# Kernel optimization log

Hardware: AMD Instinct MI355X
Metric: run time of the kernel (lower is better)

## Reference

```python
import jax, jax.numpy as jnp
import numpy as np

B, S, D_MODEL, NUM_HEADS, DFF = 4, 2048, 256, 8, 1024
DEPTH = D_MODEL // NUM_HEADS
EPS = 1e-6
LENGTH_SCALE = 1.0


def setup_inputs() -> dict:
    key = jax.random.key(0)
    ks = jax.random.split(key, 18)
    n = lambda k, shp, s=0.05: (jax.random.normal(k, shp, dtype=jnp.float32) * s)
    return {
        "x": jax.random.normal(ks[0], (B, S, D_MODEL), dtype=jnp.float32),
        "wq_w": n(ks[1], (D_MODEL, D_MODEL)), "wq_b": jnp.zeros((D_MODEL,), jnp.float32),
        "wk_w": n(ks[2], (D_MODEL, D_MODEL)), "wk_b": jnp.zeros((D_MODEL,), jnp.float32),
        "wv_w": n(ks[3], (D_MODEL, D_MODEL)), "wv_b": jnp.zeros((D_MODEL,), jnp.float32),
        "wo_w": n(ks[4], (D_MODEL, D_MODEL)), "wo_b": jnp.zeros((D_MODEL,), jnp.float32),
        "ffn1_w": n(ks[5], (D_MODEL, DFF)), "ffn1_b": jnp.zeros((DFF,), jnp.float32),
        "ffn2_w": n(ks[6], (DFF, D_MODEL)), "ffn2_b": jnp.zeros((D_MODEL,), jnp.float32),
        "ln1_g": jnp.ones((D_MODEL,), jnp.float32), "ln1_b": jnp.zeros((D_MODEL,), jnp.float32),
        "ln2_g": jnp.ones((D_MODEL,), jnp.float32), "ln2_b": jnp.zeros((D_MODEL,), jnp.float32),
    }


def _layernorm(x, g, b):
    mu = jnp.mean(x, axis=-1, keepdims=True)
    var = jnp.mean(jnp.square(x - mu), axis=-1, keepdims=True)
    return (x - mu) * jax.lax.rsqrt(var + EPS) * g + b


def _split_heads(t):
    # [B,S,D_MODEL] -> [B,H,S,depth]
    return t.reshape(B, S, NUM_HEADS, DEPTH).transpose(0, 2, 1, 3)


def _encoder_layer(x, wq_w, wq_b, wk_w, wk_b, wv_w, wv_b, wo_w, wo_b,
                   ffn1_w, ffn1_b, ffn2_w, ffn2_b, ln1_g, ln1_b, ln2_g, ln2_b):
    q = _split_heads(x @ wq_w + wq_b)
    k = _split_heads(x @ wk_w + wk_b)
    v = _split_heads(x @ wv_w + wv_b)
    # pairwise squared distances: ||q||^2 - 2 q.k + ||k||^2 -> [B,H,S,S]
    q2 = jnp.sum(q * q, axis=-1)  # [B,H,S]
    k2 = jnp.sum(k * k, axis=-1)  # [B,H,S]
    dists = q2[..., :, None] - 2.0 * jnp.einsum("bhqd,bhkd->bhqk", q, k) + k2[..., None, :]
    # exponentiated-quadratic kernel, then softmax over keys (mask=None)
    attn = jax.nn.softmax(jnp.exp(-0.5 * dists / (LENGTH_SCALE ** 2)), axis=-1)
    out = jnp.einsum("bhqk,bhkd->bhqd", attn, v)  # [B,H,S,depth]
    out = out.transpose(0, 2, 1, 3).reshape(B, S, D_MODEL)
    attn_out = out @ wo_w + wo_b
    # dropout is identity (training=False)
    out1 = _layernorm(x + attn_out, ln1_g, ln1_b)
    ffn = jax.nn.relu(out1 @ ffn1_w + ffn1_b) @ ffn2_w + ffn2_b
    return _layernorm(out1 + ffn, ln2_g, ln2_b)


def reference(x, wq_w, wq_b, wk_w, wk_b, wv_w, wv_b, wo_w, wo_b,
              ffn1_w, ffn1_b, ffn2_w, ffn2_b, ln1_g, ln1_b, ln2_g, ln2_b):
    return _encoder_layer(x, wq_w, wq_b, wk_w, wk_b, wv_w, wv_b, wo_w, wo_b,
                          ffn1_w, ffn1_b, ffn2_w, ffn2_b, ln1_g, ln1_b, ln2_g, ln2_b)
```

## Files before the change

### kernel.cpp

```cpp
#include <hip/hip_runtime.h>
#include <hip/hip_bf16.h>

#define SQL  2048
#define DM   256
#define LNEPS 1e-6f
#define NLOG2E_H (-0.72134752f)
#define LOG2E    (1.44269504f)

#define B_XB    (0ull)
#define B_QB    (4ull<<20)
#define B_KB    (8ull<<20)
#define B_VT    (12ull<<20)
#define B_CTX   (16ull<<20)
#define B_O1B   (20ull<<20)
#define B_O1F   (24ull<<20)
#define B_MID   (32ull<<20)
#define B_WQKVT (48ull<<20)
#define B_WOT   ((48ull<<20)+(512ull<<10))
#define B_W1T   (49ull<<20)
#define B_W2T   ((49ull<<20)+(512ull<<10))
#define B_BQKV  (50ull<<20)
#define B_HQ    ((50ull<<20)+(64ull<<10))
#define B_HK    ((50ull<<20)+(320ull<<10))
#define B_C2    (0ull)

typedef float  f32x16 __attribute__((ext_vector_type(16)));
typedef short  bf16x8 __attribute__((ext_vector_type(8)));
typedef int    i32x4  __attribute__((ext_vector_type(4)));
typedef int    i32x2  __attribute__((ext_vector_type(2)));

static __device__ __forceinline__ unsigned short bfu(float f){
    __hip_bfloat16 h = __float2bfloat16(f);
    return *reinterpret_cast<unsigned short*>(&h);
}
static __device__ __forceinline__ unsigned pk2(float a, float b){
    return (unsigned)bfu(a) | ((unsigned)bfu(b) << 16);
}
static __device__ __forceinline__ void glds16(const void* g, void* l){
    __builtin_amdgcn_global_load_lds((const __attribute__((address_space(1))) unsigned int*)g,
                                     (__attribute__((address_space(3))) unsigned int*)l, 16, 0, 0);
}

__global__ __launch_bounds__(256) void k_packall(
    const float* __restrict__ wq, const float* __restrict__ wk, const float* __restrict__ wv,
    const float* __restrict__ wo, const float* __restrict__ w1, const float* __restrict__ w2,
    const float* __restrict__ bq, const float* __restrict__ bk, const float* __restrict__ bv,
    const float* __restrict__ x,
    unsigned short* __restrict__ wqkvT, unsigned short* __restrict__ woT,
    unsigned short* __restrict__ w1T, unsigned short* __restrict__ w2T,
    float* __restrict__ bqkv, unsigned short* __restrict__ xb)
{
    __shared__ float tile[32][33];
    const int bid = blockIdx.x;
    const int t = threadIdx.x;
    if (bid < 768) {
        const float* W; unsigned short* Wt; int K, N, xk, yn;
        if (bid < 192) {
            int which = bid >> 6, local = bid & 63;
            W = (which == 0) ? wq : (which == 1 ? wk : wv);
            Wt = wqkvT + which * 65536; K = 256; N = 256;
            xk = local & 7; yn = local >> 3;
        } else if (bid < 256) {
            int local = bid - 192; W = wo; Wt = woT; K = 256; N = 256;
            xk = local & 7; yn = local >> 3;
        } else if (bid < 512) {
            int local = bid - 256; W = w1; Wt = w1T; K = 256; N = 1024;
            xk = local & 7; yn = local >> 3;
        } else {
            int local = bid - 512; W = w2; Wt = w2T; K = 1024; N = 256;
            xk = local & 31; yn = local >> 5;
        }
        const int tx = t & 31, ty = t >> 5;
        const int kb = xk * 32, nb = yn * 32;
#pragma unroll
        for (int i = 0; i < 32; i += 8) tile[ty + i][tx] = W[(size_t)(kb + ty + i) * N + nb + tx];
        __syncthreads();
#pragma unroll
        for (int i = 0; i < 32; i += 8) Wt[(size_t)(nb + ty + i) * K + kb + tx] = bfu(tile[tx][ty + i]);
    } else if (bid < 771) {
        int wb = bid - 768;
        const float* s = (wb == 0) ? bq : (wb == 1 ? bk : bv);
        bqkv[wb * 256 + t] = s[t];
    } else {
        const int i = (bid - 771) * 256 + t;
        float4 v = ((const float4*)x)[i];
        ushort4 o; o.x = bfu(v.x); o.y = bfu(v.y); o.z = bfu(v.z); o.w = bfu(v.w);
        ((ushort4*)xb)[i] = o;
    }
}

__global__ __launch_bounds__(256, 2) void k_qkv(
    const unsigned short* __restrict__ A, const unsigned short* __restrict__ Bt,
    const float* __restrict__ bias,
    unsigned short* __restrict__ qb, unsigned short* __restrict__ kb,
    char* __restrict__ vtg)
{
    __shared__ __align__(16) char As[16384];
    __shared__ __align__(16) char Bs[16384];
    const int t = threadIdx.x;
    const int lane = t & 63, w = t >> 6;
    const int lo = lane & 31, hi = lane >> 5;
    const int row0 = blockIdx.x * 128;
    const int col0 = blockIdx.y * 128;
    f32x16 acc[2][2] = {};
    const int gS = lane & 7;

    for (int kt = 0; kt < 4; ++kt) {
        const int k0 = kt * 64;
#pragma unroll
        for (int i = 0; i < 4; ++i) {
            const int r = w * 32 + i * 8 + (lane >> 3);
            glds16((const char*)(A  + (size_t)(row0 + r) * 256 + k0) + ((gS ^ (r & 7)) << 4),
                   As + w * 4096 + i * 1024 + lane * 16);
            glds16((const char*)(Bt + (size_t)(col0 + r) * 256 + k0) + ((gS ^ (r & 7)) << 4),
                   Bs + w * 4096 + i * 1024 + lane * 16);
        }
        __syncthreads();
        const int rA = (w >> 1) * 64 + lo;
        const int rB = (w & 1) * 64 + lo;
#pragma unroll
        for (int s = 0; s < 4; ++s) {
            const int g = s * 2 + hi;
            bf16x8 fa0 = *(const bf16x8*)(As + rA * 128 + ((g ^ (rA & 7)) << 4));
            bf16x8 fa1 = *(const bf16x8*)(As + (rA + 32) * 128 + ((g ^ (rA & 7)) << 4));
            bf16x8 fb0 = *(const bf16x8*)(Bs + rB * 128 + ((g ^ (rB & 7)) << 4));
            bf16x8 fb1 = *(const bf16x8*)(Bs + (rB + 32) * 128 + ((g ^ (rB & 7)) << 4));
            acc[0][0] = __builtin_amdgcn_mfma_f32_32x32x16_bf16(fa0, fb0, acc[0][0], 0, 0, 0);
            acc[0][1] = __builtin_amdgcn_mfma_f32_32x32x16_bf16(fa0, fb1, acc[0][1], 0, 0, 0);
            acc[1][0] = __builtin_amdgcn_mfma_f32_32x32x16_bf16(fa1, fb0, acc[1][0], 0, 0, 0);
            acc[1][1] = __builtin_amdgcn_mfma_f32_32x32x16_bf16(fa1, fb1, acc[1][1], 0, 0, 0);
        }
        __syncthreads();
    }
#pragma unroll
    for (int m = 0; m < 2; ++m)
#pragma unroll
    for (int n = 0; n < 2; ++n) {
        const int c0 = col0 + (w & 1) * 64 + n * 32;
        const int which = c0 >> 8, h = (c0 >> 5) & 7;
        const float bv = bias[c0 + lo];
        if (which < 2) {
            unsigned short* dst = (which == 0) ? qb : kb;
#pragma unroll
            for (int r = 0; r < 16; ++r) {
                const int gr = row0 + (w >> 1) * 64 + m * 32 + (r & 3) + 8 * (r >> 2) + 4 * hi;
                const int b = gr >> 11, s = gr & 2047;
                dst[(((size_t)(b * 8 + h)) * SQL + s) * 32 + lo] = bfu(acc[m][n][r] + bv);
            }
        } else {
#pragma unroll
            for (int r = 0; r < 16; ++r) {
                const int gr = row0 + (w >> 1) * 64 + m * 32 + (r & 3) + 8 * (r >> 2) + 4 * hi;
                const int b = gr >> 11, s = gr & 2047;
                const int o = s * 2;
                const int op = (o & ~0x78) | ((((o >> 3) & 15) ^ (lo & 15)) << 3);
                *(unsigned short*)(vtg + ((size_t)(b * 8 + h)) * 131072 + (size_t)lo * 4096 + op)
                    = bfu(acc[m][n][r] + bv);
            }
        }
    }
}

__global__ __launch_bounds__(256) void k_h2(const unsigned short* __restrict__ qb,
                                            const unsigned short* __restrict__ kb,
                                            float* __restrict__ hq, float* __restrict__ hk)
{
    const int gid = blockIdx.x * 256 + threadIdx.x;
    const unsigned short* qp = qb + (size_t)gid * 32;
    const unsigned short* kp = kb + (size_t)gid * 32;
    float sq = 0.f, sk = 0.f;
#pragma unroll
    for (int i = 0; i < 4; ++i) {
        i32x4 qv = *(const i32x4*)(qp + i * 8);
        i32x4 kv = *(const i32x4*)(kp + i * 8);
#pragma unroll
        for (int j = 0; j < 4; ++j) {
            unsigned int qw = (unsigned int)qv[j], kw = (unsigned int)kv[j];
            float a = __builtin_bit_cast(float, qw << 16);
            float c = __builtin_bit_cast(float, qw & 0xffff0000u);
            float d = __builtin_bit_cast(float, kw << 16);
            float e = __builtin_bit_cast(float, kw & 0xffff0000u);
            sq += a * a + c * c; sk += d * d + e * e;
        }
    }
    hq[gid] = NLOG2E_H * sq;
    hk[gid] = NLOG2E_H * sk;
}

__global__ __launch_bounds__(512, 4) void k_attn(
    const unsigned short* __restrict__ qg, const unsigned short* __restrict__ kg,
    const char* __restrict__ vtg, const float* __restrict__ hq,
    const float* __restrict__ hk, unsigned short* __restrict__ ctxb)
{
    __shared__ __align__(16) char kls[8192];
    __shared__ __align__(16) char vtl[8192];
    __shared__ __align__(16) float hks[128];
    __shared__ __align__(16) float redacc[16 * 256];
    __shared__ __align__(16) float redden[256];
    __shared__ __align__(16) float invs[128];

    const int t = threadIdx.x;
    const int grp = t >> 8;
    const int tl = t & 255;
    const int lane = t & 63;
    const int wv_ = tl >> 6;
    const int lo = lane & 31;
    const int hi = lane >> 5;

    const int bid = blockIdx.x;
    const int qchunk = bid & 15;
    const int bh = bid >> 4;

    const int qrow = qchunk * 128 + wv_ * 32 + lo;
    const unsigned short* qp = qg + ((size_t)bh * SQL + qrow) * 32;
    bf16x8 qf[2];
    qf[0] = *(const bf16x8*)(qp + hi * 8);
    qf[1] = *(const bf16x8*)(qp + 16 + hi * 8);
    const float hqv = hq[(size_t)bh * SQL + qrow];

    f32x16 acc = {};
    float den = 0.f;

    const unsigned short* kbg = kg + (size_t)bh * SQL * 32;
    const char* vtb = vtg + (size_t)bh * 131072;
    char* kd = kls + grp * 4096;
    char* vd = vtl + grp * 4096;

    for (int kt = 0; kt < 16; ++kt) {
        const int key0 = grp * 1024 + kt * 64;
        {
            const int r = tl >> 2, gl = tl & 3;
            glds16((const char*)(kbg + (size_t)(key0 + r) * 32) + ((gl ^ ((r >> 1) & 3)) << 4),
                   kd + tl * 16);
            const int vrw = tl >> 3, vch = tl & 7;
            glds16(vtb + (size_t)vrw * 4096 + key0 * 2 + vch * 16, vd + tl * 16);
            if (tl < 64) hks[grp * 64 + tl] = hk[(size_t)bh * SQL + key0 + tl];
        }
        __syncthreads();

#pragma unroll
        for (int h2 = 0; h2 < 2; ++h2) {
            const int kb32 = h2 * 32;
            const int kA = kb32 + lo;
            const char* krow = kd + kA * 64;
            const int ksw = (kA >> 1) & 3;
            bf16x8 kf0 = *(const bf16x8*)(krow + (((0 + hi) ^ ksw) << 4));
            bf16x8 kf1 = *(const bf16x8*)(krow + (((2 + hi) ^ ksw) << 4));
            f32x16 sc = {};
            sc = __builtin_amdgcn_mfma_f32_32x32x16_bf16(kf0, qf[0], sc, 0, 0, 0);
            sc = __builtin_amdgcn_mfma_f32_32x32x16_bf16(kf1, qf[1], sc, 0, 0, 0);
            const float* hb = &hks[grp * 64 + kb32];
            float4 h0 = *(const float4*)&hb[4 * hi];
            float4 h1 = *(const float4*)&hb[8 + 4 * hi];
            float4 h2v = *(const float4*)&hb[16 + 4 * hi];
            float4 h3 = *(const float4*)&hb[24 + 4 * hi];
            float hkv[16] = {h0.x,h0.y,h0.z,h0.w, h1.x,h1.y,h1.z,h1.w,
                             h2v.x,h2v.y,h2v.z,h2v.w, h3.x,h3.y,h3.z,h3.w};
            float w[16];
#pragma unroll
            for (int r = 0; r < 16; ++r) {
                float arg = fmaf(sc[r], LOG2E, hqv + hkv[r]);
                float e1  = __builtin_amdgcn_exp2f(arg);
                float ww  = __builtin_amdgcn_exp2f(e1 * LOG2E);
                den += ww;
                w[r] = ww;
            }
            i32x4 p0; p0[0]=pk2(w[0],w[1]);  p0[1]=pk2(w[2],w[3]);
                      p0[2]=pk2(w[4],w[5]);  p0[3]=pk2(w[6],w[7]);
            i32x4 p1; p1[0]=pk2(w[8],w[9]);  p1[1]=pk2(w[10],w[11]);
                      p1[2]=pk2(w[12],w[13]); p1[3]=pk2(w[14],w[15]);
            const char* vrow = vd + lo * 128;
            const int vxor = (lo & 15) << 3;
            const int o0 = (kb32 + 4 * hi) * 2;
            const int o1 = (kb32 + 16 + 4 * hi) * 2;
            i32x2 a0 = *(const i32x2*)(vrow + (o0 ^ vxor));
            i32x2 a1 = *(const i32x2*)(vrow + ((o0 + 16) ^ vxor));
            i32x2 b0 = *(const i32x2*)(vrow + (o1 ^ vxor));
            i32x2 b1 = *(const i32x2*)(vrow + ((o1 + 16) ^ vxor));
            i32x4 vb0; vb0[0]=a0[0]; vb0[1]=a0[1]; vb0[2]=a1[0]; vb0[3]=a1[1];
            i32x4 vb1; vb1[0]=b0[0]; vb1[1]=b0[1]; vb1[2]=b1[0]; vb1[3]=b1[1];
            acc = __builtin_amdgcn_mfma_f32_32x32x16_bf16(
                __builtin_bit_cast(bf16x8, p0), __builtin_bit_cast(bf16x8, vb0), acc, 0, 0, 0);
            acc = __builtin_amdgcn_mfma_f32_32x32x16_bf16(
                __builtin_bit_cast(bf16x8, p1), __builtin_bit_cast(bf16x8, vb1), acc, 0, 0, 0);
        }
        __syncthreads();
    }

    if (grp == 1) {
#pragma unroll
        for (int r = 0; r < 16; ++r) redacc[r * 256 + tl] = acc[r];
        redden[tl] = den;
    }
    __syncthreads();
    if (grp == 0) {
#pragma unroll
        for (int r = 0; r < 16; ++r) acc[r] += redacc[r * 256 + tl];
        den += redden[tl];
    }
    const float dfull = den + __shfl_xor(den, 32);
    if (grp == 0 && hi == 0) invs[wv_ * 32 + lo] = 1.f / dfull;
    __syncthreads();
    if (grp == 0) {
        float4 i0 = *(const float4*)&invs[wv_ * 32 + 4 * hi];
        float4 i1 = *(const float4*)&invs[wv_ * 32 + 8 + 4 * hi];
        float4 i2 = *(const float4*)&invs[wv_ * 32 + 16 + 4 * hi];
        float4 i3 = *(const float4*)&invs[wv_ * 32 + 24 + 4 * hi];
        float iv[16] = {i0.x,i0.y,i0.z,i0.w, i1.x,i1.y,i1.z,i1.w,
                        i2.x,i2.y,i2.z,i2.w, i3.x,i3.y,i3.z,i3.w};
        const int b = bh >> 3, h = bh & 7;
        unsigned short* cbase = ctxb + ((size_t)(b * SQL + qchunk * 128 + wv_ * 32)) * 256 + h * 32 + lo;
#pragma unroll
        for (int r = 0; r < 16; ++r) {
            const int qr = (r & 3) + 8 * (r >> 2) + 4 * hi;
            cbase[(size_t)qr * 256] = bfu(acc[r] * iv[r]);
        }
    }
}

template<int KSTRIDE, int KHALF, int NFULL, int RELU, int OUTF, int OUTB>
__global__ __launch_bounds__(256, 2) void k_gemm(
    const unsigned short* __restrict__ A, const unsigned short* __restrict__ Bt,
    const float* __restrict__ bias,
    float* __restrict__ outf, unsigned short* __restrict__ outb)
{
    __shared__ __align__(16) char As[16384];
    __shared__ __align__(16) char Bs[16384];
    const int t = threadIdx.x;
    const int lane = t & 63, w = t >> 6;
    const int lo = lane & 31, hi = lane >> 5;
    const int row0 = blockIdx.x * 128;
    const int col0 = blockIdx.y * 128;
    const int z = blockIdx.z;
    f32x16 acc[2][2] = {};
    const int gS = lane & 7;

    for (int kt = 0; kt < KHALF; ++kt) {
        const int k0 = (z * KHALF + kt) * 64;
#pragma unroll
        for (int i = 0; i < 4; ++i) {
            const int r = w * 32 + i * 8 + (lane >> 3);
            glds16((const char*)(A  + (size_t)(row0 + r) * KSTRIDE + k0) + ((gS ^ (r & 7)) << 4),
                   As + w * 4096 + i * 1024 + lane * 16);
            glds16((const char*)(Bt + (size_t)(col0 + r) * KSTRIDE + k0) + ((gS ^ (r & 7)) << 4),
                   Bs + w * 4096 + i * 1024 + lane * 16);
        }
        __syncthreads();
        const int rA = (w >> 1) * 64 + lo;
        const int rB = (w & 1) * 64 + lo;
#pragma unroll
        for (int s = 0; s < 4; ++s) {
            const int g = s * 2 + hi;
            bf16x8 fa0 = *(const bf16x8*)(As + rA * 128 + ((g ^ (rA & 7)) << 4));
            bf16x8 fa1 = *(const bf16x8*)(As + (rA + 32) * 128 + ((g ^ (rA & 7)) << 4));
            bf16x8 fb0 = *(const bf16x8*)(Bs + rB * 128 + ((g ^ (rB & 7)) << 4));
            bf16x8 fb1 = *(const bf16x8*)(Bs + (rB + 32) * 128 + ((g ^ (rB & 7)) << 4));
            acc[0][0] = __builtin_amdgcn_mfma_f32_32x32x16_bf16(fa0, fb0, acc[0][0], 0, 0, 0);
            acc[0][1] = __builtin_amdgcn_mfma_f32_32x32x16_bf16(fa0, fb1, acc[0][1], 0, 0, 0);
            acc[1][0] = __builtin_amdgcn_mfma_f32_32x32x16_bf16(fa1, fb0, acc[1][0], 0, 0, 0);
            acc[1][1] = __builtin_amdgcn_mfma_f32_32x32x16_bf16(fa1, fb1, acc[1][1], 0, 0, 0);
        }
        __syncthreads();
    }
#pragma unroll
    for (int m = 0; m < 2; ++m)
#pragma unroll
    for (int n = 0; n < 2; ++n) {
        const int c0 = col0 + (w & 1) * 64 + n * 32;
        const float bv = (z == 0) ? bias[c0 + lo] : 0.f;
#pragma unroll
        for (int r = 0; r < 16; ++r) {
            const int gr = row0 + (w >> 1) * 64 + m * 32 + (r & 3) + 8 * (r >> 2) + 4 * hi;
            float vv = acc[m][n][r] + bv;
            if (RELU) vv = fmaxf(vv, 0.f);
            if (OUTF) outf[(size_t)z * 8192 * NFULL + (size_t)gr * NFULL + c0 + lo] = vv;
            if (OUTB) outb[(size_t)gr * NFULL + c0 + lo] = bfu(vv);
        }
    }
}

template<int DUAL>
__global__ __launch_bounds__(256) void k_lnsum(
    const float* __restrict__ pa, const float* __restrict__ pb,
    const float* __restrict__ res, const float* __restrict__ g,
    const float* __restrict__ bt, float* __restrict__ outf,
    unsigned short* __restrict__ outb)
{
    const int row = blockIdx.x * 4 + (threadIdx.x >> 6);
    const int lane = threadIdx.x & 63;
    const size_t base = (size_t)row * 256;
    float4 v  = ((const float4*)(pa + base))[lane];
    float4 v2 = ((const float4*)(pb + base))[lane];
    float4 v3 = ((const float4*)(res + base))[lane];
    v.x += v2.x + v3.x; v.y += v2.y + v3.y; v.z += v2.z + v3.z; v.w += v2.w + v3.w;
    float s  = v.x + v.y + v.z + v.w;
    float ss = v.x * v.x + v.y * v.y + v.z * v.z + v.w * v.w;
#pragma unroll
    for (int off = 32; off; off >>= 1) { s += __shfl_xor(s, off); ss += __shfl_xor(ss, off); }
    const float mu = s * (1.f / 256.f);
    const float rstd = rsqrtf(ss * (1.f / 256.f) - mu * mu + LNEPS);
    const float4 gg = ((const float4*)g)[lane];
    const float4 bb = ((const float4*)bt)[lane];
    float4 o;
    o.x = (v.x - mu) * rstd * gg.x + bb.x;
    o.y = (v.y - mu) * rstd * gg.y + bb.y;
    o.z = (v.z - mu) * rstd * gg.z + bb.z;
    o.w = (v.w - mu) * rstd * gg.w + bb.w;
    ((float4*)(outf + base))[lane] = o;
    if (DUAL) {
        ushort4 ob; ob.x = bfu(o.x); ob.y = bfu(o.y); ob.z = bfu(o.z); ob.w = bfu(o.w);
        ((ushort4*)(outb + base))[lane] = ob;
    }
}

extern "C" void kernel_launch(void* const* d_in, const int* in_sizes, int n_in,
                              void* d_out, int out_size, void* d_ws, size_t ws_size,
                              hipStream_t stream) {
    const float* x   = (const float*)d_in[0];
    const float* wq  = (const float*)d_in[1];  const float* bq  = (const float*)d_in[2];
    const float* wk  = (const float*)d_in[3];  const float* bk  = (const float*)d_in[4];
    const float* wv  = (const float*)d_in[5];  const float* bv  = (const float*)d_in[6];
    const float* wo  = (const float*)d_in[7];  const float* wob = (const float*)d_in[8];
    const float* w1  = (const float*)d_in[9];  const float* b1  = (const float*)d_in[10];
    const float* w2  = (const float*)d_in[11]; const float* b2  = (const float*)d_in[12];
    const float* g1  = (const float*)d_in[13]; const float* bl1 = (const float*)d_in[14];
    const float* g2  = (const float*)d_in[15]; const float* bl2 = (const float*)d_in[16];

    char* ws = (char*)d_ws;
    unsigned short* xb    = (unsigned short*)(ws + B_XB);
    unsigned short* qb    = (unsigned short*)(ws + B_QB);
    unsigned short* kbuf  = (unsigned short*)(ws + B_KB);
    char*           vt    = (char*)(ws + B_VT);
    unsigned short* ctxb  = (unsigned short*)(ws + B_CTX);
    unsigned short* o1b   = (unsigned short*)(ws + B_O1B);
    float*          o1f   = (float*)(ws + B_O1F);
    unsigned short* mid   = (unsigned short*)(ws + B_MID);
    float*          c1    = (float*)(ws + B_MID);
    float*          c2    = (float*)(ws + B_C2);
    unsigned short* wqkvT = (unsigned short*)(ws + B_WQKVT);
    unsigned short* woT   = (unsigned short*)(ws + B_WOT);
    unsigned short* w1T   = (unsigned short*)(ws + B_W1T);
    unsigned short* w2T   = (unsigned short*)(ws + B_W2T);
    float* bqkv = (float*)(ws + B_BQKV);
    float* hqb  = (float*)(ws + B_HQ);
    float* hkb  = (float*)(ws + B_HK);
    float* out  = (float*)d_out;

    k_packall<<<dim3(2819), dim3(256), 0, stream>>>(wq, wk, wv, wo, w1, w2, bq, bk, bv, x,
                                                    wqkvT, woT, w1T, w2T, bqkv, xb);
    k_qkv<<<dim3(64, 6), dim3(256), 0, stream>>>(xb, wqkvT, bqkv, qb, kbuf, vt);
    k_h2<<<dim3(256), dim3(256), 0, stream>>>(qb, kbuf, hqb, hkb);
    k_attn<<<dim3(512), dim3(512), 0, stream>>>(qb, kbuf, vt, hqb, hkb, ctxb);
    k_gemm<256, 2, 256, 0, 1, 0><<<dim3(64, 2, 2), dim3(256), 0, stream>>>(ctxb, woT, wob, c1, nullptr);
    k_lnsum<1><<<dim3(2048), dim3(256), 0, stream>>>(c1, c1 + 2097152, x, g1, bl1, o1f, o1b);
    k_gemm<256, 4, 1024, 1, 0, 1><<<dim3(64, 8, 1), dim3(256), 0, stream>>>(o1b, w1T, b1, nullptr, mid);
    k_gemm<1024, 8, 256, 0, 1, 0><<<dim3(64, 2, 2), dim3(256), 0, stream>>>(mid, w2T, b2, c2, nullptr);
    k_lnsum<0><<<dim3(2048), dim3(256), 0, stream>>>(c2, c2 + 2097152, o1f, g2, bl2, out, nullptr);
}
```

Before: 199.2 us.

## Double-buffer GEMM tiles, fold norms into MFMA, split attention into four key groups

The QKV and generic GEMM kernels now double-buffer their LDS tiles, issuing the next tile's loads before computing the current one and dropping one barrier per iteration. Attention folds the squared-norm bias terms into an extra MFMA with a ones/bias augmented operand, and pre-scales Q by log2(e) so the inner loop no longer needs FMAs or per-key norm loads. The attention grid is reorganised to 64 query rows per block with four key groups of 128 threads, doubling the block count, followed by a three-way cross-group reduction. The trade-offs are more LDS per block (64 KB for the GEMMs, which may lower occupancy), the precision of the norms rounded to bf16 inside the MFMA, and a possible race: in the double-buffered loop the next stage is issued without a barrier before the buffer is reused.

```diff
diff --git a/kernel.cpp b/kernel.cpp
--- a/kernel.cpp
+++ b/kernel.cpp
@@ -4,7 +4,6 @@
 #define SQL  2048
 #define DM   256
 #define LNEPS 1e-6f
-#define NLOG2E_H (-0.72134752f)
 #define LOG2E    (1.44269504f)
 
 #define B_XB    (0ull)
@@ -95,8 +94,7 @@
     unsigned short* __restrict__ qb, unsigned short* __restrict__ kb,
     char* __restrict__ vtg)
 {
-    __shared__ __align__(16) char As[16384];
-    __shared__ __align__(16) char Bs[16384];
+    __shared__ __align__(16) char smem[65536];
     const int t = threadIdx.x;
     const int lane = t & 63, w = t >> 6;
     const int lo = lane & 31, hi = lane >> 5;
@@ -104,18 +102,28 @@
     const int col0 = blockIdx.y * 128;
     f32x16 acc[2][2] = {};
     const int gS = lane & 7;
-
-    for (int kt = 0; kt < 4; ++kt) {
+    const int rr = w * 32 + (lane >> 3);
+
+    auto stage = [&](int buf, int kt) {
         const int k0 = kt * 64;
+        char* As = smem + buf * 32768;
+        char* Bs = As + 16384;
 #pragma unroll
         for (int i = 0; i < 4; ++i) {
-            const int r = w * 32 + i * 8 + (lane >> 3);
+            const int r = rr + i * 8;
             glds16((const char*)(A  + (size_t)(row0 + r) * 256 + k0) + ((gS ^ (r & 7)) << 4),
                    As + w * 4096 + i * 1024 + lane * 16);
             glds16((const char*)(Bt + (size_t)(col0 + r) * 256 + k0) + ((gS ^ (r & 7)) << 4),
                    Bs + w * 4096 + i * 1024 + lane * 16);
         }
-        __syncthreads();
+    };
+
+    stage(0, 0);
+    __syncthreads();
+    for (int kt = 0; kt < 4; ++kt) {
+        if (kt + 1 < 4) stage((kt + 1) & 1, kt + 1);
+        const char* As = smem + (kt & 1) * 32768;
+        const char* Bs = As + 16384;
         const int rA = (w >> 1) * 64 + lo;
         const int rB = (w & 1) * 64 + lo;
 #pragma unroll
@@ -141,11 +149,12 @@
         const float bv = bias[c0 + lo];
         if (which < 2) {
             unsigned short* dst = (which == 0) ? qb : kb;
+            const float scl = (which == 0) ? LOG2E : 1.0f;
 #pragma unroll
             for (int r = 0; r < 16; ++r) {
                 const int gr = row0 + (w >> 1) * 64 + m * 32 + (r & 3) + 8 * (r >> 2) + 4 * hi;
                 const int b = gr >> 11, s = gr & 2047;
-                dst[(((size_t)(b * 8 + h)) * SQL + s) * 32 + lo] = bfu(acc[m][n][r] + bv);
+                dst[(((size_t)(b * 8 + h)) * SQL + s) * 32 + lo] = bfu((acc[m][n][r] + bv) * scl);
             }
         } else {
 #pragma unroll
@@ -183,8 +192,8 @@
             sq += a * a + c * c; sk += d * d + e * e;
         }
     }
-    hq[gid] = NLOG2E_H * sq;
-    hk[gid] = NLOG2E_H * sk;
+    hq[gid] = -0.34657359f * sq + 0.52876637f;
+    hk[gid] = -0.72134752f * sk;
 }
 
 __global__ __launch_bounds__(512, 4) void k_attn(
@@ -192,31 +201,34 @@
     const char* __restrict__ vtg, const float* __restrict__ hq,
     const float* __restrict__ hk, unsigned short* __restrict__ ctxb)
 {
-    __shared__ __align__(16) char kls[8192];
-    __shared__ __align__(16) char vtl[8192];
-    __shared__ __align__(16) float hks[128];
-    __shared__ __align__(16) float redacc[16 * 256];
-    __shared__ __align__(16) float redden[256];
-    __shared__ __align__(16) float invs[128];
+    __shared__ __align__(16) char kls[16384];
+    __shared__ __align__(16) char vtl[16384];
+    __shared__ __align__(16) float hks[256];
+    __shared__ __align__(16) float redacc[3 * 16 * 128];
+    __shared__ __align__(16) float redden[3 * 128];
+    __shared__ __align__(16) float invs[64];
 
     const int t = threadIdx.x;
-    const int grp = t >> 8;
-    const int tl = t & 255;
+    const int grp = t >> 7;
+    const int tl  = t & 127;
     const int lane = t & 63;
-    const int wv_ = tl >> 6;
+    const int w   = (t >> 6) & 1;
     const int lo = lane & 31;
     const int hi = lane >> 5;
 
     const int bid = blockIdx.x;
-    const int qchunk = bid & 15;
-    const int bh = bid >> 4;
-
-    const int qrow = qchunk * 128 + wv_ * 32 + lo;
+    const int qc = bid & 31;
+    const int bh = bid >> 5;
+
+    const int qrow = qc * 64 + w * 32 + lo;
     const unsigned short* qp = qg + ((size_t)bh * SQL + qrow) * 32;
-    bf16x8 qf[2];
-    qf[0] = *(const bf16x8*)(qp + hi * 8);
-    qf[1] = *(const bf16x8*)(qp + 16 + hi * 8);
+    bf16x8 qf0 = *(const bf16x8*)(qp + hi * 8);
+    bf16x8 qf1 = *(const bf16x8*)(qp + 16 + hi * 8);
     const float hqv = hq[(size_t)bh * SQL + qrow];
+
+    i32x4 b3i = {};
+    if (hi == 0) b3i[0] = 0x3F80u | ((unsigned)bfu(hqv) << 16);
+    const bf16x8 b3 = __builtin_bit_cast(bf16x8, b3i);
 
     f32x16 acc = {};
     float den = 0.f;
@@ -226,14 +238,18 @@
     char* kd = kls + grp * 4096;
     char* vd = vtl + grp * 4096;
 
-    for (int kt = 0; kt < 16; ++kt) {
-        const int key0 = grp * 1024 + kt * 64;
+    for (int kt = 0; kt < 8; ++kt) {
+        const int key0 = grp * 512 + kt * 64;
         {
-            const int r = tl >> 2, gl = tl & 3;
-            glds16((const char*)(kbg + (size_t)(key0 + r) * 32) + ((gl ^ ((r >> 1) & 3)) << 4),
-                   kd + tl * 16);
-            const int vrw = tl >> 3, vch = tl & 7;
-            glds16(vtb + (size_t)vrw * 4096 + key0 * 2 + vch * 16, vd + tl * 16);
+#pragma unroll
+            for (int it = 0; it < 2; ++it) {
+                const int idx = it * 128 + tl;
+                const int r = idx >> 2, gl = idx & 3;
+                glds16((const char*)(kbg + (size_t)(key0 + r) * 32) + ((gl ^ ((r >> 1) & 3)) << 4),
+                       kd + idx * 16);
+                const int vrw = idx >> 3, vch = idx & 7;
+                glds16(vtb + (size_t)vrw * 4096 + key0 * 2 + vch * 16, vd + idx * 16);
+            }
             if (tl < 64) hks[grp * 64 + tl] = hk[(size_t)bh * SQL + key0 + tl];
         }
         __syncthreads();
@@ -246,29 +262,25 @@
             const int ksw = (kA >> 1) & 3;
             bf16x8 kf0 = *(const bf16x8*)(krow + (((0 + hi) ^ ksw) << 4));
             bf16x8 kf1 = *(const bf16x8*)(krow + (((2 + hi) ^ ksw) << 4));
+            i32x4 a3i = {};
+            if (hi == 0) a3i[0] = (unsigned)bfu(hks[grp * 64 + kA]) | 0x3F800000u;
             f32x16 sc = {};
-            sc = __builtin_amdgcn_mfma_f32_32x32x16_bf16(kf0, qf[0], sc, 0, 0, 0);
-            sc = __builtin_amdgcn_mfma_f32_32x32x16_bf16(kf1, qf[1], sc, 0, 0, 0);
-            const float* hb = &hks[grp * 64 + kb32];
-            float4 h0 = *(const float4*)&hb[4 * hi];
-            float4 h1 = *(const float4*)&hb[8 + 4 * hi];
-            float4 h2v = *(const float4*)&hb[16 + 4 * hi];
-            float4 h3 = *(const float4*)&hb[24 + 4 * hi];
-            float hkv[16] = {h0.x,h0.y,h0.z,h0.w, h1.x,h1.y,h1.z,h1.w,
-                             h2v.x,h2v.y,h2v.z,h2v.w, h3.x,h3.y,h3.z,h3.w};
-            float w[16];
+            sc = __builtin_amdgcn_mfma_f32_32x32x16_bf16(kf0, qf0, sc, 0, 0, 0);
+            sc = __builtin_amdgcn_mfma_f32_32x32x16_bf16(kf1, qf1, sc, 0, 0, 0);
+            sc = __builtin_amdgcn_mfma_f32_32x32x16_bf16(
+                     __builtin_bit_cast(bf16x8, a3i), b3, sc, 0, 0, 0);
+            float wv[16];
 #pragma unroll
             for (int r = 0; r < 16; ++r) {
-                float arg = fmaf(sc[r], LOG2E, hqv + hkv[r]);
-                float e1  = __builtin_amdgcn_exp2f(arg);
-                float ww  = __builtin_amdgcn_exp2f(e1 * LOG2E);
+                float e1 = __builtin_amdgcn_exp2f(sc[r]);
+                float ww = __builtin_amdgcn_exp2f(e1);
                 den += ww;
-                w[r] = ww;
+                wv[r] = ww;
             }
-            i32x4 p0; p0[0]=pk2(w[0],w[1]);  p0[1]=pk2(w[2],w[3]);
-                      p0[2]=pk2(w[4],w[5]);  p0[3]=pk2(w[6],w[7]);
-            i32x4 p1; p1[0]=pk2(w[8],w[9]);  p1[1]=pk2(w[10],w[11]);
-                      p1[2]=pk2(w[12],w[13]); p1[3]=pk2(w[14],w[15]);
+            i32x4 p0; p0[0]=pk2(wv[0],wv[1]);   p0[1]=pk2(wv[2],wv[3]);
+                      p0[2]=pk2(wv[4],wv[5]);   p0[3]=pk2(wv[6],wv[7]);
+            i32x4 p1; p1[0]=pk2(wv[8],wv[9]);   p1[1]=pk2(wv[10],wv[11]);
+                      p1[2]=pk2(wv[12],wv[13]); p1[3]=pk2(wv[14],wv[15]);
             const char* vrow = vd + lo * 128;
             const int vxor = (lo & 15) << 3;
             const int o0 = (kb32 + 4 * hi) * 2;
@@ -287,29 +299,27 @@
         __syncthreads();
     }
 
-    if (grp == 1) {
-#pragma unroll
-        for (int r = 0; r < 16; ++r) redacc[r * 256 + tl] = acc[r];
-        redden[tl] = den;
+    if (grp != 0) {
+#pragma unroll
+        for (int r = 0; r < 16; ++r) redacc[((grp - 1) * 16 + r) * 128 + tl] = acc[r];
+        redden[(grp - 1) * 128 + tl] = den;
     }
     __syncthreads();
     if (grp == 0) {
 #pragma unroll
-        for (int r = 0; r < 16; ++r) acc[r] += redacc[r * 256 + tl];
-        den += redden[tl];
-    }
-    const float dfull = den + __shfl_xor(den, 32);
-    if (grp == 0 && hi == 0) invs[wv_ * 32 + lo] = 1.f / dfull;
-    __syncthreads();
-    if (grp == 0) {
-        float4 i0 = *(const float4*)&invs[wv_ * 32 + 4 * hi];
-        float4 i1 = *(const float4*)&invs[wv_ * 32 + 8 + 4 * hi];
-        float4 i2 = *(const float4*)&invs[wv_ * 32 + 16 + 4 * hi];
-        float4 i3 = *(const float4*)&invs[wv_ * 32 + 24 + 4 * hi];
+        for (int r = 0; r < 16; ++r)
+            acc[r] += redacc[r * 128 + tl] + redacc[(16 + r) * 128 + tl] + redacc[(32 + r) * 128 + tl];
+        den += redden[tl] + redden[128 + tl] + redden[256 + tl];
+        const float dfull = den + __shfl_xor(den, 32);
+        if (hi == 0) invs[w * 32 + lo] = 1.f / dfull;
+        float4 i0 = *(const float4*)&invs[w * 32 + 4 * hi];
+        float4 i1 = *(const float4*)&invs[w * 32 + 8 + 4 * hi];
+        float4 i2 = *(const float4*)&invs[w * 32 + 16 + 4 * hi];
+        float4 i3 = *(const float4*)&invs[w * 32 + 24 + 4 * hi];
         float iv[16] = {i0.x,i0.y,i0.z,i0.w, i1.x,i1.y,i1.z,i1.w,
                         i2.x,i2.y,i2.z,i2.w, i3.x,i3.y,i3.z,i3.w};
         const int b = bh >> 3, h = bh & 7;
-        unsigned short* cbase = ctxb + ((size_t)(b * SQL + qchunk * 128 + wv_ * 32)) * 256 + h * 32 + lo;
+        unsigned short* cbase = ctxb + ((size_t)(b * SQL + qc * 64 + w * 32)) * 256 + h * 32 + lo;
 #pragma unroll
         for (int r = 0; r < 16; ++r) {
             const int qr = (r & 3) + 8 * (r >> 2) + 4 * hi;
@@ -318,14 +328,13 @@
     }
 }
 
-template<int KSTRIDE, int KHALF, int NFULL, int RELU, int OUTF, int OUTB>
+template<int KSTRIDE, int KT, int NFULL, int RELU, int OUTF, int OUTB>
 __global__ __launch_bounds__(256, 2) void k_gemm(
     const unsigned short* __restrict__ A, const unsigned short* __restrict__ Bt,
     const float* __restrict__ bias,
     float* __restrict__ outf, unsigned short* __restrict__ outb)
 {
-    __shared__ __align__(16) char As[16384];
-    __shared__ __align__(16) char Bs[16384];
+    __shared__ __align__(16) char smem[65536];
     const int t = threadIdx.x;
     const int lane = t & 63, w = t >> 6;
     const int lo = lane & 31, hi = lane >> 5;
@@ -334,18 +343,28 @@
     const int z = blockIdx.z;
     f32x16 acc[2][2] = {};
     const int gS = lane & 7;
-
-    for (int kt = 0; kt < KHALF; ++kt) {
-        const int k0 = (z * KHALF + kt) * 64;
+    const int rr = w * 32 + (lane >> 3);
+
+    auto stage = [&](int buf, int kt) {
+        const int k0 = (z * KT + kt) * 64;
+        char* As = smem + buf * 32768;
+        char* Bs = As + 16384;
 #pragma unroll
         for (int i = 0; i < 4; ++i) {
-            const int r = w * 32 + i * 8 + (lane >> 3);
+            const int r = rr + i * 8;
             glds16((const char*)(A  + (size_t)(row0 + r) * KSTRIDE + k0) + ((gS ^ (r & 7)) << 4),
                    As + w * 4096 + i * 1024 + lane * 16);
             glds16((const char*)(Bt + (size_t)(col0 + r) * KSTRIDE + k0) + ((gS ^ (r & 7)) << 4),
                    Bs + w * 4096 + i * 1024 + lane * 16);
         }
-        __syncthreads();
+    };
+
+    stage(0, 0);
+    __syncthreads();
+    for (int kt = 0; kt < KT; ++kt) {
+        if (kt + 1 < KT) stage((kt + 1) & 1, kt + 1);
+        const char* As = smem + (kt & 1) * 32768;
+        const char* Bs = As + 16384;
         const int rA = (w >> 1) * 64 + lo;
         const int rB = (w & 1) * 64 + lo;
 #pragma unroll
@@ -450,7 +469,7 @@
                                                     wqkvT, woT, w1T, w2T, bqkv, xb);
     k_qkv<<<dim3(64, 6), dim3(256), 0, stream>>>(xb, wqkvT, bqkv, qb, kbuf, vt);
     k_h2<<<dim3(256), dim3(256), 0, stream>>>(qb, kbuf, hqb, hkb);
-    k_attn<<<dim3(512), dim3(512), 0, stream>>>(qb, kbuf, vt, hqb, hkb, ctxb);
+    k_attn<<<dim3(1024), dim3(512), 0, stream>>>(qb, kbuf, vt, hqb, hkb, ctxb);
     k_gemm<256, 2, 256, 0, 1, 0><<<dim3(64, 2, 2), dim3(256), 0, stream>>>(ctxb, woT, wob, c1, nullptr);
     k_lnsum<1><<<dim3(2048), dim3(256), 0, stream>>>(c1, c1 + 2097152, x, g1, bl1, o1f, o1b);
     k_gemm<256, 4, 1024, 1, 0, 1><<<dim3(64, 8, 1), dim3(256), 0, stream>>>(o1b, w1T, b1, nullptr, mid);
```

New measurement: 195.3 us. Within noise of the previous version (-1.9%).
